# Performance work log

Hardware: AMD Instinct MI355X
Metric: run time of the kernel (lower is better)

The kernel has to match this reference:

```python
import jax, jax.numpy as jnp
import numpy as np

HIDDEN = 2048
NUM_HEADS = 16
HEAD_DIM = HIDDEN // NUM_HEADS  # 128
BATCH = 2
SEQ = 2048
ROPE_BASE = 10000.0


def _rope_cos_sin(seq_len, dim):
    inv_freq = 1.0 / (ROPE_BASE ** (jnp.arange(0, dim, 2, dtype=jnp.float32) / dim))
    t = jnp.arange(seq_len, dtype=jnp.float32)
    freqs = jnp.outer(t, inv_freq)              # [S, dim/2]
    emb = jnp.concatenate([freqs, freqs], -1)   # [S, dim]
    return jnp.cos(emb), jnp.sin(emb)


def _rotate_half(x):
    x1, x2 = jnp.split(x, 2, axis=-1)
    return jnp.concatenate([-x2, x1], axis=-1)


def setup_inputs() -> dict:
    key = jax.random.key(0)
    k1, k2, k3 = jax.random.split(key, 3)
    hidden_states = jax.random.normal(k1, (BATCH, SEQ, HIDDEN), dtype=jnp.float32)
    Wqkv = jax.random.normal(k2, (3 * HIDDEN, HIDDEN), dtype=jnp.float32) * (1.0 / np.sqrt(HIDDEN))
    Wout = jax.random.normal(k3, (HIDDEN, HIDDEN), dtype=jnp.float32) * (1.0 / np.sqrt(HIDDEN))
    causal = jnp.tril(jnp.ones((SEQ, SEQ), dtype=bool))
    attention_mask = jnp.where(causal, 0.0, -1e9).astype(jnp.float32)[None, None]  # [1,1,S,S]
    return {"hidden_states": hidden_states, "attention_mask": attention_mask,
            "Wqkv": Wqkv, "Wout": Wout}


def reference(hidden_states, attention_mask, Wqkv, Wout):
    B, S, H = hidden_states.shape
    # fused QKV projection (torch Linear: x @ W.T)
    qkv = hidden_states @ Wqkv.T                                   # [B,S,3H]
    qkv = qkv.reshape(B, S, 3, NUM_HEADS, HEAD_DIM)
    qkv = jnp.transpose(qkv, (2, 0, 3, 1, 4))                      # [3,B,nh,S,hd]
    q, k, v = qkv[0], qkv[1], qkv[2]
    # RoPE
    cos, sin = _rope_cos_sin(S, HEAD_DIM)                          # [S,hd]
    q = q * cos + _rotate_half(q) * sin
    k = k * cos + _rotate_half(k) * sin
    # attention
    scale = jnp.sqrt(jnp.float32(HEAD_DIM))
    scores = jnp.einsum('bhqd,bhkd->bhqk', q, k) / scale           # [B,nh,S,S]
    scores = scores + attention_mask
    attn = jax.nn.softmax(scores, axis=-1)
    out = jnp.einsum('bhqk,bhkd->bhqd', attn, v)                   # [B,nh,S,hd]
    out = jnp.transpose(out, (0, 2, 1, 3)).reshape(B, S, H)
    return out @ Wout.T
```

## Files before the change

kernel.cpp:

```cpp
#include <hip/hip_runtime.h>
#include <cmath>

using u16 = unsigned short;
typedef __bf16 bf16x8 __attribute__((ext_vector_type(8)));
typedef float f32x4 __attribute__((ext_vector_type(4)));
typedef u16 u16x4 __attribute__((ext_vector_type(4)));
typedef u16 u16x8 __attribute__((ext_vector_type(8)));

#define HIDDEN 2048
#define NH 16
#define HD 128
#define BATCH 2
#define SEQ 2048
#define TOKENS 4096
#define NQKV 6144
#define CSC 0.12751744f

__device__ __forceinline__ u16 f2bf(float f) {
  union { __bf16 h; u16 u; } cv; cv.h = (__bf16)f; return cv.u;
}
__device__ __forceinline__ float bf2f(u16 u) {
  union { __bf16 h; u16 u; } cv; cv.u = u; return (float)cv.h;
}
__device__ __forceinline__ void gload16(const void* g, void* l) {
  __builtin_amdgcn_global_load_lds(
      (const __attribute__((address_space(1))) unsigned int*)g,
      (__attribute__((address_space(3))) unsigned int*)l, 16, 0, 0);
}

__global__ __launch_bounds__(256) void cvt3_kernel(
    const float* __restrict__ x, const float* __restrict__ wq,
    const float* __restrict__ wo, u16* __restrict__ xb,
    u16* __restrict__ wqb, u16* __restrict__ wob) {
  int i = blockIdx.x * 256 + threadIdx.x;
  const float* in;
  u16* out;
  if (i < 1048576) {
    in = x; out = xb;
  } else if (i < 1048576 + 1572864) {
    i -= 1048576; in = wq; out = wqb;
  } else {
    i -= 1048576 + 1572864; in = wo; out = wob;
  }
  const float4* p = (const float4*)(in + (size_t)i * 8);
  float4 f0 = p[0], f1 = p[1];
  u16x8 u;
  u[0] = f2bf(f0.x); u[1] = f2bf(f0.y); u[2] = f2bf(f0.z); u[3] = f2bf(f0.w);
  u[4] = f2bf(f1.x); u[5] = f2bf(f1.y); u[6] = f2bf(f1.z); u[7] = f2bf(f1.w);
  *(u16x8*)(out + (size_t)i * 8) = u;
}

__global__ void rope_table_kernel(float* __restrict__ ct, float* __restrict__ st) {
  int idx = blockIdx.x * blockDim.x + threadIdx.x;
  if (idx >= SEQ * 64) return;
  int s = idx >> 6, i = idx & 63;
  float invf = 1.0f / powf(10000.0f, (2.0f * (float)i) / 128.0f);
  float ang = (float)s * invf;
  ct[idx] = cosf(ang);
  st[idx] = sinf(ang);
}

template <int MODE>
__global__ __launch_bounds__(256) void gemm_bf16(
    const u16* __restrict__ A, const u16* __restrict__ B,
    int M, int N, int K, float* __restrict__ C,
    u16* __restrict__ qbv, u16* __restrict__ kbv, u16* __restrict__ vtb,
    const float* __restrict__ ct, const float* __restrict__ st) {
  __shared__ u16 As[2][128 * 64];
  __shared__ u16 Bs[2][128 * 64];
  const int tid = threadIdx.x;
  const int l = tid & 63, w = tid >> 6;
  const int wm = w >> 1, wn = w & 1;
  const int lin = blockIdx.x + blockIdx.y * gridDim.x;
  const int nwg = gridDim.x * gridDim.y;
  const int swz = (lin & 7) * (nwg >> 3) + (lin >> 3);
  const int m0 = (swz & 31) * 128;
  const int n0 = (swz >> 5) * 128;
  const int lr8 = l >> 3, lc8 = l & 7;
  const int lg = l >> 4, lm = l & 15;
  f32x4 acc[4][4] = {};

  auto STAGE = [&](int bsel, int k0) {
#pragma unroll
    for (int c4 = 0; c4 < 4; ++c4) {
      int c = w * 4 + c4;
      int row = c * 8 + lr8;
      int se = 8 * (lc8 ^ (row & 7));
      gload16(A + (size_t)(m0 + row) * K + k0 + se, &As[bsel][c * 512 + l * 8]);
      gload16(B + (size_t)(n0 + row) * K + k0 + se, &Bs[bsel][c * 512 + l * 8]);
    }
  };

  const int NT = K >> 6;
  STAGE(0, 0);
  __syncthreads();
  int cur = 0;

  for (int t = 0; t < NT; ++t) {
    if (t + 1 < NT) STAGE(cur ^ 1, (t + 1) << 6);
    __builtin_amdgcn_s_setprio(1);
#pragma unroll
    for (int kk = 0; kk < 2; ++kk) {
      int ko = kk * 32 + lg * 8;
      bf16x8 af[4], bfr[4];
#pragma unroll
      for (int f = 0; f < 4; ++f) {
        int m = wm * 64 + f * 16 + lm;
        af[f] = *(const bf16x8*)&As[cur][m * 64 + (ko ^ ((m & 7) * 8))];
        int n = f * 32 + wn * 16 + lm;
        bfr[f] = *(const bf16x8*)&Bs[cur][n * 64 + (ko ^ ((n & 7) * 8))];
      }
#pragma unroll
      for (int i = 0; i < 4; ++i)
#pragma unroll
        for (int j = 0; j < 4; ++j)
          acc[i][j] = __builtin_amdgcn_mfma_f32_16x16x32_bf16(af[i], bfr[j], acc[i][j], 0, 0, 0);
    }
    __builtin_amdgcn_s_setprio(0);
    __syncthreads();
    cur ^= 1;
  }

#pragma unroll
  for (int i = 0; i < 4; ++i) {
    int mrow0 = m0 + wm * 64 + i * 16 + lg * 4;
    if (MODE == 0) {
#pragma unroll
      for (int j = 0; j < 4; ++j) {
        int n = n0 + j * 32 + wn * 16 + lm;
#pragma unroll
        for (int r = 0; r < 4; ++r)
          C[(size_t)(mrow0 + r) * N + n] = acc[i][j][r];
      }
    } else if (n0 >= 4096) {
      const int hh = (n0 & 2047) >> 7;
      const int bb = mrow0 >> 11, s = mrow0 & 2047;
#pragma unroll
      for (int j = 0; j < 4; ++j) {
        int d = j * 32 + wn * 16 + lm;
        u16x4 pv;
#pragma unroll
        for (int r = 0; r < 4; ++r) pv[r] = f2bf(acc[i][j][r]);
        *(u16x4*)(vtb + ((size_t)((bb * NH + hh) * HD + d)) * SEQ + s) = pv;
      }
    } else {
      const int qk = n0 >> 11;
      const int hh = (n0 & 2047) >> 7;
      u16* dst = qk ? kbv : qbv;
      const float scl = qk ? 1.0f : CSC;
#pragma unroll
      for (int r = 0; r < 4; ++r) {
        int t = mrow0 + r;
        int b = t >> 11, s = t & 2047;
        const float* cb = ct + s * 64 + wn * 16 + lm;
        const float* sb = st + s * 64 + wn * 16 + lm;
        float c0 = cb[0], c1 = cb[32], s0 = sb[0], s1 = sb[32];
        u16* row = dst + ((size_t)(b * NH + hh) * SEQ + s) * HD + wn * 16 + lm;
#pragma unroll
        for (int j = 0; j < 4; ++j) {
          float cv = (j & 1) ? c1 : c0;
          float sv = (j & 1) ? s1 : s0;
          float x = acc[i][j][r], xp = acc[i][j ^ 2][r];
          float ov = (j < 2) ? (x * cv - xp * sv) : (x * cv + xp * sv);
          row[j * 32] = f2bf(ov * scl);
        }
      }
    }
  }
}

__global__ __launch_bounds__(256) void attn_kernel(
    const u16* __restrict__ qb, const u16* __restrict__ kb,
    const u16* __restrict__ vtb, u16* __restrict__ aob) {
  __shared__ u16 Ks[2][64 * 128];
  __shared__ u16 Vts[2][128 * 64];
  __shared__ u16 Ps[64 * 72];
  const int tid = threadIdx.x;
  const int l = tid & 63, w = tid >> 6;
  const int lg = l >> 4, lm = l & 15;
  const int bh = blockIdx.y;
  const int qp = blockIdx.x;
  const u16* qbase = qb + (size_t)bh * SEQ * HD;
  const u16* kbase = kb + (size_t)bh * SEQ * HD;
  const u16* vbase = vtb + (size_t)bh * HD * SEQ;
  const int b = bh >> 4, h = bh & 15;

  auto STAGE = [&](int bsel, int k0) {
#pragma unroll
    for (int c4 = 0; c4 < 4; ++c4) {
      int c = w * 4 + c4;
      { int row = c * 4 + lg;
        int se = 8 * (lm ^ (row & 15));
        gload16(kbase + (size_t)(k0 + row) * HD + se, &Ks[bsel][c * 512 + l * 8]); }
      { int row = c * 8 + (l >> 3);
        int se = 8 * ((l & 7) ^ (row & 7));
        gload16(vbase + (size_t)row * SEQ + k0 + se, &Vts[bsel][c * 512 + l * 8]); }
    }
  };

#pragma unroll 1
  for (int pass = 0; pass < 2; ++pass) {
    const int qt = pass ? (31 - qp) : qp;
    const int q0 = qt * 64;
    const int nkt = qt + 1;

    const int qrow = w * 16 + lm;
    bf16x8 qf[4];
#pragma unroll
    for (int kk = 0; kk < 4; ++kk)
      qf[kk] = *(const bf16x8*)(qbase + (size_t)(q0 + qrow) * HD + kk * 32 + lg * 8);

    f32x4 o[8] = {};
    float l_p[4] = {0.0f, 0.0f, 0.0f, 0.0f};

    STAGE(0, 0);
    __syncthreads();
    int cur = 0;

    for (int kt = 0; kt < nkt; ++kt) {
      if (kt + 1 < nkt) STAGE(cur ^ 1, (kt + 1) * 64);

      f32x4 sc[4] = {};
      __builtin_amdgcn_s_setprio(1);
#pragma unroll
      for (int kk = 0; kk < 4; ++kk) {
        int ko = kk * 32 + lg * 8;
#pragma unroll
        for (int fn = 0; fn < 4; ++fn) {
          int krow = fn * 16 + lm;
          bf16x8 bb = *(const bf16x8*)&Ks[cur][krow * 128 + (ko ^ ((krow & 15) * 8))];
          sc[fn] = __builtin_amdgcn_mfma_f32_16x16x32_bf16(qf[kk], bb, sc[fn], 0, 0, 0);
        }
      }
      __builtin_amdgcn_s_setprio(0);

      if (kt == nkt - 1) {
        const int k0 = kt * 64;
#pragma unroll
        for (int fn = 0; fn < 4; ++fn) {
          int kg = k0 + fn * 16 + lm;
#pragma unroll
          for (int r = 0; r < 4; ++r) {
            int qg = q0 + w * 16 + lg * 4 + r;
            if (kg > qg) sc[fn][r] = -3.0e38f;
          }
        }
      }

#pragma unroll
      for (int r = 0; r < 4; ++r) {
        float psum = 0.0f;
#pragma unroll
        for (int fn = 0; fn < 4; ++fn) {
          float p = __builtin_amdgcn_exp2f(sc[fn][r] - 8.0f);
          psum += p;
          Ps[(w * 16 + lg * 4 + r) * 72 + fn * 16 + lm] = f2bf(p);
        }
        l_p[r] += psum;
      }

      const int prow = w * 16 + lm;
      __builtin_amdgcn_s_setprio(1);
#pragma unroll
      for (int ks = 0; ks < 2; ++ks) {
        int ko = ks * 32 + lg * 8;
        bf16x8 pa = *(const bf16x8*)&Ps[prow * 72 + ko];
#pragma unroll
        for (int f8 = 0; f8 < 8; ++f8) {
          int d = f8 * 16 + lm;
          bf16x8 vv = *(const bf16x8*)&Vts[cur][d * 64 + (ko ^ ((d & 7) * 8))];
          o[f8] = __builtin_amdgcn_mfma_f32_16x16x32_bf16(pa, vv, o[f8], 0, 0, 0);
        }
      }
      __builtin_amdgcn_s_setprio(0);

      __syncthreads();
      cur ^= 1;
    }

    float inv[4];
#pragma unroll
    for (int r = 0; r < 4; ++r) {
      float v = l_p[r];
#pragma unroll
      for (int off = 1; off < 16; off <<= 1) v += __shfl_xor(v, off, 16);
      inv[r] = 1.0f / v;
    }
#pragma unroll
    for (int f8 = 0; f8 < 8; ++f8) {
      int d = h * 128 + f8 * 16 + lm;
#pragma unroll
      for (int r = 0; r < 4; ++r) {
        int s = q0 + w * 16 + lg * 4 + r;
        aob[(size_t)(b * SEQ + s) * HIDDEN + d] = f2bf(o[f8][r] * inv[r]);
      }
    }
    __syncthreads();
  }
}

extern "C" void kernel_launch(void* const* d_in, const int* in_sizes, int n_in,
                              void* d_out, int out_size, void* d_ws, size_t ws_size,
                              hipStream_t stream) {
  const float* x = (const float*)d_in[0];
  const float* Wqkv = (const float*)d_in[2];
  const float* Wout = (const float*)d_in[3];
  float* out = (float*)d_out;

  char* ws = (char*)d_ws;
  u16* xb  = (u16*)(ws + 0);
  u16* wqb = (u16*)(ws + 16777216);
  u16* wob = (u16*)(ws + 41943040);
  u16* qbv = (u16*)(ws + 50331648);
  u16* kbv = (u16*)(ws + 67108864);
  u16* vtb = (u16*)(ws + 83886080);
  u16* aob = (u16*)(ws + 100663296);
  float* ct = (float*)(ws + 117440512);
  float* st = (float*)(ws + 117964800);

  cvt3_kernel<<<12288, 256, 0, stream>>>(x, Wqkv, Wout, xb, wqb, wob);
  rope_table_kernel<<<512, 256, 0, stream>>>(ct, st);

  gemm_bf16<1><<<dim3(48, 32), 256, 0, stream>>>(xb, wqb, TOKENS, NQKV, HIDDEN,
                                                 nullptr, qbv, kbv, vtb, ct, st);
  attn_kernel<<<dim3(16, 32), 256, 0, stream>>>(qbv, kbv, vtb, aob);
  gemm_bf16<0><<<dim3(16, 32), 256, 0, stream>>>(aob, wob, TOKENS, HIDDEN, HIDDEN,
                                                 out, nullptr, nullptr, nullptr, nullptr, nullptr);
}
```

Measured before the change: 379.4 us.

## Replace QKV GEMM with 256x256 tile, 8-wave ping-pong pipelined kernel

Adds a dedicated QKV projection kernel that uses 256x256 output tiles, 512 threads (8 waves), a double-buffered split-half LDS layout and a four-phase interleaving of LDS reads, global prefetch and MFMA with explicit vmcnt waits and barriers. The epilogue is remapped so each tile covers two heads, with RoPE pairing moved to the j^1 fragment. Larger tiles cut global/LDS traffic per FLOP and the phased schedule aims to overlap loads with MFMA. The cost is higher register and LDS pressure (128KB LDS) and more barriers, and with 384 blocks on 256 CUs the wave count is uneven.

New measurement: 410.5 us. +8.2%, slower.

```diff
diff --git a/kernel.cpp b/kernel.cpp
--- a/kernel.cpp
+++ b/kernel.cpp
@@ -60,12 +60,133 @@
   st[idx] = sinf(ang);
 }
 
+__global__ __launch_bounds__(512, 2) void gemm_qkv_8p(
+    const u16* __restrict__ A, const u16* __restrict__ B,
+    u16* __restrict__ qbv, u16* __restrict__ kbv, u16* __restrict__ vtb,
+    const float* __restrict__ ct, const float* __restrict__ st) {
+  __shared__ u16 Ah[2][2][128 * 64];
+  __shared__ u16 Bh[2][2][128 * 64];
+  const int tid = threadIdx.x;
+  const int l = tid & 63, w = tid >> 6;
+  const int lg = l >> 4, lm = l & 15;
+  const int wr = w >> 2, wc = w & 3;
+  const int K = HIDDEN;
+  const int lin = blockIdx.x;
+  const int swz = (lin & 7) * 48 + (lin >> 3);
+  const int m0 = (swz & 15) * 256;
+  const int n0 = (swz >> 4) * 256;
+
+  const int srow = tid >> 3;
+  const int sse = 8 * ((tid & 7) ^ (srow & 7));
+  auto STG = [&](const u16* src, u16* lds, int gr0, int k0) {
+    gload16(src + (size_t)(gr0 + srow) * K + k0 + sse, lds + tid * 8);
+    gload16(src + (size_t)(gr0 + srow + 64) * K + k0 + sse, lds + tid * 8 + 4096);
+  };
+
+  f32x4 acc[8][4] = {};
+
+  STG(A, &Ah[0][0][0], m0, 0);       STG(A, &Ah[0][1][0], m0 + 128, 0);
+  STG(B, &Bh[0][0][0], n0, 0);       STG(B, &Bh[0][1][0], n0 + 128, 0);
+  STG(A, &Ah[1][0][0], m0, 64);      STG(A, &Ah[1][1][0], m0 + 128, 64);
+  STG(B, &Bh[1][0][0], n0, 64);      STG(B, &Bh[1][1][0], n0 + 128, 64);
+  asm volatile("s_waitcnt vmcnt(8)" ::: "memory");
+  __builtin_amdgcn_s_barrier();
+
+  const int sxor = (lm & 7) * 8;
+  bf16x8 af[4][2], bfv[4][2];
+
+  for (int kt = 0; kt < 32; ++kt) {
+    const int buf = kt & 1;
+#pragma unroll
+    for (int p = 0; p < 4; ++p) {
+      const int mh = p >> 1, nh = p & 1;
+      if (p == 0 || p == 2) {
+#pragma unroll
+        for (int f = 0; f < 4; ++f) {
+          const int hr = mh * 64 + f * 16 + lm;
+#pragma unroll
+          for (int kk = 0; kk < 2; ++kk)
+            af[f][kk] = *(const bf16x8*)&Ah[buf][wr][hr * 64 + ((kk * 32 + lg * 8) ^ sxor)];
+        }
+      }
+      if (p < 2) {
+#pragma unroll
+        for (int jj = 0; jj < 2; ++jj) {
+          const int hrb = wc * 16 + jj * 64 + lm;
+#pragma unroll
+          for (int kk = 0; kk < 2; ++kk)
+            bfv[nh * 2 + jj][kk] = *(const bf16x8*)&Bh[buf][nh][hrb * 64 + ((kk * 32 + lg * 8) ^ sxor)];
+        }
+      }
+      if (p == 2 && kt + 2 < 32) {
+        STG(B, &Bh[buf][0][0], n0, (kt + 2) * 64);
+        STG(B, &Bh[buf][1][0], n0 + 128, (kt + 2) * 64);
+      }
+      if (p == 3 && kt + 2 < 32) {
+        STG(A, &Ah[buf][0][0], m0, (kt + 2) * 64);
+        STG(A, &Ah[buf][1][0], m0 + 128, (kt + 2) * 64);
+      }
+      __builtin_amdgcn_s_barrier();
+      __builtin_amdgcn_s_setprio(1);
+#pragma unroll
+      for (int f = 0; f < 4; ++f)
+#pragma unroll
+        for (int jj = 0; jj < 2; ++jj)
+#pragma unroll
+          for (int kk = 0; kk < 2; ++kk)
+            acc[mh * 4 + f][nh * 2 + jj] = __builtin_amdgcn_mfma_f32_16x16x32_bf16(
+                af[f][kk], bfv[nh * 2 + jj][kk], acc[mh * 4 + f][nh * 2 + jj], 0, 0, 0);
+      __builtin_amdgcn_s_setprio(0);
+      if (p == 3) {
+        if (kt + 2 < 32) { asm volatile("s_waitcnt vmcnt(8)" ::: "memory"); }
+        else if (kt + 1 < 32) { asm volatile("s_waitcnt vmcnt(0)" ::: "memory"); }
+      }
+      __builtin_amdgcn_s_barrier();
+    }
+  }
+
+  const int qkv = n0 >> 11;
+  const int h0 = (n0 & 2047) >> 7;
+#pragma unroll
+  for (int i = 0; i < 8; ++i) {
+    const int mrow0 = m0 + wr * 128 + (i >> 2) * 64 + (i & 3) * 16 + lg * 4;
+    if (qkv == 2) {
+      const int bb = mrow0 >> 11, s = mrow0 & 2047;
+#pragma unroll
+      for (int j = 0; j < 4; ++j) {
+        const int d = wc * 16 + (j & 1) * 64 + lm;
+        const int hh = h0 + (j >> 1);
+        u16x4 pv;
+#pragma unroll
+        for (int r = 0; r < 4; ++r) pv[r] = f2bf(acc[i][j][r]);
+        *(u16x4*)(vtb + ((size_t)((bb * NH + hh) * HD + d)) * SEQ + s) = pv;
+      }
+    } else {
+      u16* dst = qkv ? kbv : qbv;
+      const float scl = qkv ? 1.0f : CSC;
+#pragma unroll
+      for (int r = 0; r < 4; ++r) {
+        const int t = mrow0 + r;
+        const int b = t >> 11, s = t & 2047;
+        const float c = ct[s * 64 + wc * 16 + lm];
+        const float sn = st[s * 64 + wc * 16 + lm];
+#pragma unroll
+        for (int j = 0; j < 4; ++j) {
+          const int d = wc * 16 + (j & 1) * 64 + lm;
+          const int hh = h0 + (j >> 1);
+          float x = acc[i][j][r], xp = acc[i][j ^ 1][r];
+          float ov = ((j & 1) == 0) ? (x * c - xp * sn) : (x * c + xp * sn);
+          dst[((size_t)(b * NH + hh) * SEQ + s) * HD + d] = f2bf(ov * scl);
+        }
+      }
+    }
+  }
+}
+
 template <int MODE>
 __global__ __launch_bounds__(256) void gemm_bf16(
     const u16* __restrict__ A, const u16* __restrict__ B,
-    int M, int N, int K, float* __restrict__ C,
-    u16* __restrict__ qbv, u16* __restrict__ kbv, u16* __restrict__ vtb,
-    const float* __restrict__ ct, const float* __restrict__ st) {
+    int M, int N, int K, float* __restrict__ C) {
   __shared__ u16 As[2][128 * 64];
   __shared__ u16 Bs[2][128 * 64];
   const int tid = threadIdx.x;
@@ -124,47 +245,12 @@
 #pragma unroll
   for (int i = 0; i < 4; ++i) {
     int mrow0 = m0 + wm * 64 + i * 16 + lg * 4;
-    if (MODE == 0) {
-#pragma unroll
-      for (int j = 0; j < 4; ++j) {
-        int n = n0 + j * 32 + wn * 16 + lm;
-#pragma unroll
-        for (int r = 0; r < 4; ++r)
-          C[(size_t)(mrow0 + r) * N + n] = acc[i][j][r];
-      }
-    } else if (n0 >= 4096) {
-      const int hh = (n0 & 2047) >> 7;
-      const int bb = mrow0 >> 11, s = mrow0 & 2047;
-#pragma unroll
-      for (int j = 0; j < 4; ++j) {
-        int d = j * 32 + wn * 16 + lm;
-        u16x4 pv;
-#pragma unroll
-        for (int r = 0; r < 4; ++r) pv[r] = f2bf(acc[i][j][r]);
-        *(u16x4*)(vtb + ((size_t)((bb * NH + hh) * HD + d)) * SEQ + s) = pv;
-      }
-    } else {
-      const int qk = n0 >> 11;
-      const int hh = (n0 & 2047) >> 7;
-      u16* dst = qk ? kbv : qbv;
-      const float scl = qk ? 1.0f : CSC;
-#pragma unroll
-      for (int r = 0; r < 4; ++r) {
-        int t = mrow0 + r;
-        int b = t >> 11, s = t & 2047;
-        const float* cb = ct + s * 64 + wn * 16 + lm;
-        const float* sb = st + s * 64 + wn * 16 + lm;
-        float c0 = cb[0], c1 = cb[32], s0 = sb[0], s1 = sb[32];
-        u16* row = dst + ((size_t)(b * NH + hh) * SEQ + s) * HD + wn * 16 + lm;
-#pragma unroll
-        for (int j = 0; j < 4; ++j) {
-          float cv = (j & 1) ? c1 : c0;
-          float sv = (j & 1) ? s1 : s0;
-          float x = acc[i][j][r], xp = acc[i][j ^ 2][r];
-          float ov = (j < 2) ? (x * cv - xp * sv) : (x * cv + xp * sv);
-          row[j * 32] = f2bf(ov * scl);
-        }
-      }
+#pragma unroll
+    for (int j = 0; j < 4; ++j) {
+      int n = n0 + j * 32 + wn * 16 + lm;
+#pragma unroll
+      for (int r = 0; r < 4; ++r)
+        C[(size_t)(mrow0 + r) * N + n] = acc[i][j][r];
     }
   }
 }
@@ -321,9 +407,7 @@
   cvt3_kernel<<<12288, 256, 0, stream>>>(x, Wqkv, Wout, xb, wqb, wob);
   rope_table_kernel<<<512, 256, 0, stream>>>(ct, st);
 
-  gemm_bf16<1><<<dim3(48, 32), 256, 0, stream>>>(xb, wqb, TOKENS, NQKV, HIDDEN,
-                                                 nullptr, qbv, kbv, vtb, ct, st);
+  gemm_qkv_8p<<<384, 512, 0, stream>>>(xb, wqb, qbv, kbv, vtb, ct, st);
   attn_kernel<<<dim3(16, 32), 256, 0, stream>>>(qbv, kbv, vtb, aob);
-  gemm_bf16<0><<<dim3(16, 32), 256, 0, stream>>>(aob, wob, TOKENS, HIDDEN, HIDDEN,
-                                                 out, nullptr, nullptr, nullptr, nullptr, nullptr);
-}
+  gemm_bf16<0><<<dim3(16, 32), 256, 0, stream>>>(aob, wob, TOKENS, HIDDEN, HIDDEN, out);
+}
```
